# Optimization experiments

Hardware: AMD Instinct MI355X
Metric: run time of the kernel (lower is better)

## Reference

```python
import jax, jax.numpy as jnp
import numpy as np
import math

B, S, E, H = 4, 1024, 1024, 16
D = E // H
C = 1.0           # Poincare ball curvature
CS = math.sqrt(C)
EPS = 1e-7

def _sq(x):
    return jnp.sum(x * x, axis=-1, keepdims=True)

def expmap0(v):
    n = jnp.sqrt(jnp.clip(_sq(v), 1e-15))
    return jnp.tanh(CS * n) * v / (CS * n)

def logmap0(y):
    n = jnp.sqrt(jnp.clip(_sq(y), 1e-15))
    t = jnp.clip(CS * n, 0.0, 1.0 - 1e-6)
    return jnp.arctanh(t) * y / (CS * n)

def hlinear(x, z, r):
    # Poincare fully-connected layer (HNN++, Shimizu et al.), as in hypll HLinear
    lam = 2.0 / jnp.clip(1.0 - C * _sq(x), EPS)          # [..., 1] conformal factor
    zn = jnp.clip(jnp.linalg.norm(z, axis=0), 1e-15)     # [out]
    xz = x @ z                                           # [..., out]
    tcr = 2.0 * CS * r
    v = (2.0 * zn / CS) * jnp.arcsinh(CS * lam * xz / zn * jnp.cosh(tcr) - (lam - 1.0) * jnp.sinh(tcr))
    w = jnp.sinh(CS * v) / CS
    return w / (1.0 + jnp.sqrt(1.0 + C * jnp.sum(w * w, -1, keepdims=True)))

def _beta(a, b):
    return math.exp(math.lgamma(a) + math.lgamma(b) - math.lgamma(a + b))

def _forward(query, key, value, zq, bq, zk, bk, zv, bv):
    pq, pk, pv = hlinear(query, zq, bq), hlinear(key, zk, bk), hlinear(value, zv, bv)
    split = lambda x: x.reshape(B, S, H, D).transpose(0, 2, 1, 3)   # [B,H,S,D]
    q, k, v = split(pq), split(pk), split(pv)
    # attention_similarity: negative per-head pairwise Poincare distance (all heads vectorized)
    q2 = jnp.sum(q * q, -1)                              # [B,H,Sq]
    k2 = jnp.sum(k * k, -1)                              # [B,H,Sk]
    qk = jnp.einsum('bhqd,bhkd->bhqk', q, k)
    diff2 = jnp.clip(q2[..., :, None] + k2[..., None, :] - 2.0 * qk, 0.0)
    den = jnp.clip((1.0 - C * q2)[..., :, None] * (1.0 - C * k2)[..., None, :], EPS)
    dist = jnp.arccosh(jnp.clip(1.0 + 2.0 * C * diff2 / den, 1.0 + 1e-6)) / CS
    # attention_activation: softmax over keys
    w = jax.nn.softmax(-dist, axis=-1)                   # [B,H,Sq,Sk]
    # attention_midpoint: weighted gyromidpoint of values over keys
    lam = 2.0 / jnp.clip(1.0 - C * jnp.sum(v * v, -1), EPS)          # [B,H,Sk]
    num = jnp.einsum('bhqk,bhkd->bhqd', w * lam[..., None, :], v)
    dnm = jnp.clip(jnp.einsum('bhqk,bhk->bhq', jnp.abs(w), lam - 1.0), EPS)
    u = num / dnm[..., None]
    mid = u / (1.0 + jnp.sqrt(jnp.clip(1.0 - C * _sq(u), EPS)))      # (1/2) Mobius scalar mult
    # manifold.cat: beta-concatenation of heads (HNN++)
    scale = _beta(E / 2.0, 0.5) / _beta(D / 2.0, 0.5)
    tv = logmap0(mid) * scale                            # tangent at origin, [B,H,S,D]
    return expmap0(tv.transpose(0, 2, 1, 3).reshape(B, S, E))

def setup_inputs():
    key = jax.random.key(0)
    ks = jax.random.split(key, 9)
    mk = lambda k: expmap0(jax.random.normal(k, (B, S, E), jnp.float32) * (0.3 / math.sqrt(E)))
    zs = lambda k: jax.random.normal(k, (E, E), jnp.float32) / math.sqrt(E)
    bs = lambda k: jax.random.normal(k, (E,), jnp.float32) * 0.01
    return {"query": mk(ks[0]), "key": mk(ks[1]), "value": mk(ks[2]),
            "zq": zs(ks[3]), "bq": bs(ks[4]), "zk": zs(ks[5]), "bk": bs(ks[6]),
            "zv": zs(ks[7]), "bv": bs(ks[8])}

def reference(query, key, value, zq, bq, zk, bk, zv, bv):
    return _forward(query, key, value, zq, bq, zk, bk, zv, bv)
```

## Files before the change

### kernel.cpp

```cpp
#include <hip/hip_runtime.h>
#include <cmath>

#define EPSF 1e-7f

constexpr int B_ = 4, S_ = 1024, E_ = 1024, H_ = 16, D_ = 64;
constexpr int BS_ = B_ * S_;

typedef __attribute__((ext_vector_type(8))) short bf16x8;
typedef __attribute__((ext_vector_type(4))) float f32x4;

__device__ inline unsigned int fbits(float f) { union { float f; unsigned int u; } x; x.f = f; return x.u; }
__device__ inline float ubits(unsigned int u) { union { unsigned int u; float f; } x; x.u = u; return x.f; }

__device__ inline unsigned short f2bf(float f) {
  unsigned int u = fbits(f);
  unsigned int r = u + 0x7fffu + ((u >> 16) & 1u);
  return (unsigned short)(r >> 16);
}
__device__ inline float bf2f(unsigned short h) { return ubits(((unsigned int)h) << 16); }
__device__ inline float fastrcp(float x) { return __builtin_amdgcn_rcpf(x); }
__device__ inline float fastsqrt(float x) { return __builtin_amdgcn_sqrtf(x); }

__device__ __forceinline__ void async_ld16(const unsigned short* g, unsigned short* l) {
  __builtin_amdgcn_global_load_lds(
      (const __attribute__((address_space(1))) unsigned int*)g,
      (__attribute__((address_space(3))) unsigned int*)l, 16, 0, 0);
}

__device__ __forceinline__ unsigned int cvt_pk_bf16(float lo, float hi) {
  unsigned int r;
  asm("v_cvt_pk_bf16_f32 %0, %1, %2" : "=v"(r) : "v"(lo), "v"(hi));
  return r;
}
__device__ __forceinline__ void permlane32_swap(unsigned int &a, unsigned int &b) {
  asm("v_permlane32_swap_b32 %0, %1" : "+v"(a), "+v"(b));
}
__device__ __forceinline__ void permlane16_swap(unsigned int &a, unsigned int &b) {
  asm("v_permlane16_swap_b32 %0, %1" : "+v"(a), "+v"(b));
}

__global__ __launch_bounds__(256) void prep_kernel(
    const float* __restrict__ xq, const float* __restrict__ xk,
    const float* __restrict__ xv, unsigned short* __restrict__ Xbf,
    float* __restrict__ lamRow,
    const float* __restrict__ zq, const float* __restrict__ zk, const float* __restrict__ zv,
    unsigned short* __restrict__ BhiT, float* __restrict__ Zpart) {
  const int bid = blockIdx.x;
  const int tid = threadIdx.x;
  if (bid < 3 * BS_ / 4) {
    const int wid = tid >> 6, lane = tid & 63;
    const int row = bid * 4 + wid;
    const float* x = (row < BS_) ? xq : (row < 2 * BS_ ? xk : xv);
    const int r = row & (BS_ - 1);
    const float4* src = (const float4*)(x + (size_t)r * E_);
    float4 v[4];
    #pragma unroll
    for (int j = 0; j < 4; j++) v[j] = src[lane + 64 * j];
    float s = 0.f;
    #pragma unroll
    for (int j = 0; j < 4; j++)
      s += v[j].x * v[j].x + v[j].y * v[j].y + v[j].z * v[j].z + v[j].w * v[j].w;
    #pragma unroll
    for (int m = 1; m < 64; m <<= 1) s += __shfl_xor(s, m, 64);
    uint2* dst = (uint2*)(Xbf + (size_t)row * E_);
    #pragma unroll
    for (int j = 0; j < 4; j++) {
      uint2 p;
      p.x = (unsigned int)f2bf(v[j].x) | ((unsigned int)f2bf(v[j].y) << 16);
      p.y = (unsigned int)f2bf(v[j].z) | ((unsigned int)f2bf(v[j].w) << 16);
      dst[lane + 64 * j] = p;
    }
    if (lane == 0) lamRow[row] = 2.0f / fmaxf(1.0f - s, EPSF);
    return;
  }
  const int lid = bid - 3 * BS_ / 4;
  const int mat = lid >> 8;
  const int rem = lid & 255;
  const int ky = rem >> 4, nx = rem & 15;
  const float* z = mat == 0 ? zq : (mat == 1 ? zk : zv);
  const int k0 = ky * 64, n0 = nx * 64;
  __shared__ float t[64][65];
  __shared__ float sred[64][4];
  {
    int kr = tid >> 4, nc = (tid & 15) * 4;
    #pragma unroll
    for (int i = 0; i < 4; i++) {
      float4 vv = *(const float4*)(z + (size_t)(k0 + kr + i * 16) * E_ + n0 + nc);
      t[kr + i * 16][nc + 0] = vv.x;
      t[kr + i * 16][nc + 1] = vv.y;
      t[kr + i * 16][nc + 2] = vv.z;
      t[kr + i * 16][nc + 3] = vv.w;
    }
  }
  __syncthreads();
  int nr = tid >> 2, kc = (tid & 3) * 16;
  unsigned int ph[8];
  float ss = 0.f;
  #pragma unroll
  for (int p = 0; p < 8; p++) {
    float x0 = t[kc + 2 * p][nr], x1 = t[kc + 2 * p + 1][nr];
    ph[p] = (unsigned int)f2bf(x0) | ((unsigned int)f2bf(x1) << 16);
    ss += x0 * x0 + x1 * x1;
  }
  size_t off = (size_t)mat * E_ * E_ + (size_t)(n0 + nr) * E_ + k0 + kc;
  uint4* dh = (uint4*)(BhiT + off);
  dh[0] = make_uint4(ph[0], ph[1], ph[2], ph[3]);
  dh[1] = make_uint4(ph[4], ph[5], ph[6], ph[7]);
  sred[nr][tid & 3] = ss;
  __syncthreads();
  if (tid < 64) {
    float v = sred[tid][0] + sred[tid][1] + sred[tid][2] + sred[tid][3];
    Zpart[(size_t)(mat * 16 + ky) * E_ + n0 + tid] = v;
  }
}

__global__ __launch_bounds__(256, 3) void hlinear_mfma_kernel(
    const unsigned short* __restrict__ Xbf,
    const unsigned short* __restrict__ BhiT,
    const float* __restrict__ lamRow, const float* __restrict__ Zpart,
    const float* __restrict__ bq, const float* __restrict__ bk, const float* __restrict__ bv,
    unsigned short* __restrict__ Wbf) {
  const int fid = blockIdx.x;
  const int xcd = fid & 7, j = fid >> 3;
  const int n0 = (j & 7) * 128;
  const int gp = xcd * 12 + (j >> 3);
  const int mat = gp >> 5;
  const int m0 = (gp & 31) * 128;

  const unsigned short* xa = Xbf + (size_t)mat * BS_ * E_;
  const unsigned short* bh = BhiT + (size_t)mat * E_ * E_;

  __shared__ unsigned short LDSU[18432];
  __shared__ float chznS[128], shS[128], tznS[128];
  unsigned short* As = LDSU;
  unsigned short* Bh = LDSU + 8192;

  const int tid = threadIdx.x;
  const int wid = tid >> 6, lane = tid & 63, quad = lane >> 4, l16 = lane & 15;
  const int wm = (wid >> 1) * 64, wn = (wid & 1) * 64;

  if (tid < 128) {
    const int col = n0 + tid;
    float s = 0.f;
    #pragma unroll
    for (int ky = 0; ky < 16; ky++)
      s += Zpart[(size_t)(mat * 16 + ky) * E_ + col];
    float zn = fmaxf(sqrtf(s), 1e-15f);
    const float* bb = (mat == 0) ? bq : ((mat == 1) ? bk : bv);
    float rb = bb[col];
    chznS[tid] = coshf(2.f * rb) / zn;
    shS[tid] = sinhf(2.f * rb);
    tznS[tid] = 2.f * zn;
  }

  f32x4 acc[4][4];
  #pragma unroll
  for (int i = 0; i < 4; i++)
    #pragma unroll
    for (int jj = 0; jj < 4; jj++) acc[i][jj] = (f32x4){0.f, 0.f, 0.f, 0.f};

  const int lrow = lane >> 3;
  const int lcs = ((lane & 7) ^ lrow) * 8;
  const int xsw = (l16 & 7);

  for (int kt = 0; kt < E_ / 64; ++kt) {
    __syncthreads();
    const int kb = kt * 64 + lcs;
    #pragma unroll
    for (int c2 = 0; c2 < 4; c2++) {
      const int c = wid * 4 + c2;
      const int grow = c * 8 + lrow;
      async_ld16(xa + (size_t)(m0 + grow) * E_ + kb, As + c * 512);
      async_ld16(bh + (size_t)(n0 + grow) * E_ + kb, Bh + c * 512);
    }
    __syncthreads();
    #pragma unroll
    for (int h = 0; h < 2; h++) {
      bf16x8 a[4];
      #pragma unroll
      for (int mt = 0; mt < 4; mt++) {
        int row = wm + mt * 16 + l16;
        a[mt] = *(const bf16x8*)&As[row * 64 + (((h * 4 + quad) ^ xsw) * 8)];
      }
      #pragma unroll
      for (int nt = 0; nt < 4; nt++) {
        int row = wn + nt * 16 + l16;
        bf16x8 bhf = *(const bf16x8*)&Bh[row * 64 + (((h * 4 + quad) ^ xsw) * 8)];
        #pragma unroll
        for (int mt = 0; mt < 4; mt++)
          acc[mt][nt] = __builtin_amdgcn_mfma_f32_16x16x32_bf16(a[mt], bhf, acc[mt][nt], 0, 0, 0);
      }
    }
  }

  const float* lamP = lamRow + mat * BS_;
  float lamv[16];
  #pragma unroll
  for (int mt = 0; mt < 4; mt++)
    #pragma unroll
    for (int r = 0; r < 4; r++)
      lamv[mt * 4 + r] = lamP[m0 + wm + mt * 16 + quad * 4 + r];

  __syncthreads();
  unsigned short* epi = LDSU + wid * 4608;
  #pragma unroll
  for (int nt = 0; nt < 4; nt++) {
    int ci = wn + nt * 16 + l16;
    float chzn = chznS[ci];
    float sh = shS[ci];
    float tzn = tznS[ci];
    #pragma unroll
    for (int mt = 0; mt < 4; mt++) {
      #pragma unroll
      for (int r = 0; r < 4; r++) {
        float lam = lamv[mt * 4 + r];
        float arg = fmaf(lam * acc[mt][nt][r], chzn, -(lam - 1.f) * sh);
        float sq2 = sqrtf(fmaf(arg, arg, 1.f));
        float v = tzn * __logf(arg + sq2);
        float ev = __expf(v);
        float w = 0.5f * (ev - fastrcp(ev));
        epi[(mt * 16 + quad * 4 + r) * 72 + nt * 16 + l16] = f2bf(w);
      }
    }
  }
  unsigned short* gout = Wbf + (size_t)mat * BS_ * E_ + (size_t)(m0 + wm) * E_ + n0 + wn;
  const int rrow = lane >> 3, seg = lane & 7;
  #pragma unroll
  for (int i = 0; i < 8; i++) {
    int row = i * 8 + rrow;
    uint4 val = *(const uint4*)&epi[row * 72 + seg * 8];
    *(uint4*)(gout + (size_t)row * E_ + seg * 8) = val;
  }
}

__global__ __launch_bounds__(256) void normalize_kernel(
    const unsigned short* __restrict__ Wbf, unsigned short* __restrict__ Pbf,
    float* __restrict__ HN,
    unsigned short* __restrict__ KsG, unsigned short* __restrict__ lamMG,
    unsigned int* __restrict__ auxG) {
  const int wid = threadIdx.x >> 6, lane = threadIdx.x & 63;
  const int row = blockIdx.x * 4 + wid;
  const unsigned short* w = Wbf + (size_t)row * E_;
  union { uint4 q[2]; unsigned short s[16]; } in;
  in.q[0] = ((const uint4*)w)[lane * 2];
  in.q[1] = ((const uint4*)w)[lane * 2 + 1];
  float wv[16];
  float s = 0.f;
  #pragma unroll
  for (int i = 0; i < 16; i++) { wv[i] = bf2f(in.s[i]); s += wv[i] * wv[i]; }
  #pragma unroll
  for (int m = 1; m < 64; m <<= 1) s += __shfl_xor(s, m, 64);
  float t = 1.f / (1.f + sqrtf(1.f + s));
  union { uint4 q[2]; unsigned short s[16]; } out;
  float rv[16];
  float hs = 0.f;
  #pragma unroll
  for (int i = 0; i < 16; i++) {
    unsigned short p = f2bf(wv[i] * t);
    out.s[i] = p;
    rv[i] = bf2f(p);
    hs += rv[i] * rv[i];
  }
  hs += __shfl_xor(hs, 1, 64);
  hs += __shfl_xor(hs, 2, 64);
  const int mat = row >= 2 * BS_ ? 2 : (row >= BS_ ? 1 : 0);
  const int r4 = row & (BS_ - 1);
  const int b = r4 >> 10, key = r4 & (S_ - 1);
  const int head = lane >> 2;
  const size_t bhS = ((size_t)(b * H_ + head)) * S_;
  if (mat == 0) {
    ((uint4*)(Pbf + (size_t)row * E_))[lane * 2] = out.q[0];
    ((uint4*)(Pbf + (size_t)row * E_))[lane * 2 + 1] = out.q[1];
    if ((lane & 3) == 0) HN[(size_t)r4 * H_ + head] = hs;
  } else if (mat == 1) {
    float c = fastrcp(1.f - hs);
    union { uint4 q[2]; unsigned short s[16]; } ks;
    #pragma unroll
    for (int i = 0; i < 16; i++) ks.s[i] = f2bf(rv[i] * c);
    unsigned short* dst = KsG + (bhS + key) * 64 + (lane & 3) * 16;
    ((uint4*)dst)[0] = ks.q[0];
    ((uint4*)dst)[1] = ks.q[1];
    if ((lane & 3) == 0)
      auxG[bhS + key] = (unsigned int)f2bf(c) | ((unsigned int)f2bf(c * hs) << 16);
  } else {
    float lam = 2.f / fmaxf(1.f - hs, EPSF);
    union { uint4 q[2]; unsigned short s[16]; } pv;
    #pragma unroll
    for (int i = 0; i < 16; i++) pv.s[i] = f2bf(rv[i] * lam);
    ((uint4*)(Pbf + (size_t)row * E_))[lane * 2] = pv.q[0];
    ((uint4*)(Pbf + (size_t)row * E_))[lane * 2 + 1] = pv.q[1];
    if ((lane & 3) == 0) lamMG[bhS + key] = f2bf(lam - 1.f);
  }
}

__global__ __launch_bounds__(256) void vtrans_kernel(
    const unsigned short* __restrict__ PvF, unsigned short* __restrict__ VtG) {
  const int st = blockIdx.x, h = blockIdx.y, b = blockIdx.z;
  __shared__ unsigned short T[64][72];
  const int tid = threadIdx.x;
  const size_t bhS = (size_t)(b * H_ + h) * S_;
  {
    int lr = tid >> 2, lc = (tid & 3) * 16;
    const uint4* src = (const uint4*)(PvF + (size_t)(b * S_ + st * 64 + lr) * E_ + h * 64 + lc);
    *(uint4*)&T[lr][lc] = src[0];
    *(uint4*)&T[lr][lc + 8] = src[1];
  }
  __syncthreads();
  int d = tid >> 2, sc = (tid & 3) * 16;
  unsigned int o[8];
  #pragma unroll
  for (int i = 0; i < 8; i++) {
    int s0 = sc + 2 * i;
    o[i] = (unsigned int)T[s0][d] | ((unsigned int)T[s0 + 1][d] << 16);
  }
  unsigned short* dst = VtG + bhS * 64 + (size_t)d * S_ + st * 64 + sc;
  ((uint4*)dst)[0] = make_uint4(o[0], o[1], o[2], o[3]);
  ((uint4*)dst)[1] = make_uint4(o[4], o[5], o[6], o[7]);
}

__global__ __launch_bounds__(512) void attention_kernel(
    const unsigned short* __restrict__ Pbf, const float* __restrict__ HN,
    const unsigned short* __restrict__ KsG, const unsigned short* __restrict__ VtG,
    const unsigned short* __restrict__ lamMG, const unsigned int* __restrict__ auxG,
    float* __restrict__ TV, float scale) {
  const int fid = blockIdx.x;
  const int xcd = fid & 7, slot = fid >> 3;
  const int group = xcd + 8 * (slot >> 3);
  const int qt = slot & 7;
  const int h = group & 15, b = group >> 4;

  const unsigned short* pq = Pbf;
  const float* hnq = HN;

  const int tid = threadIdx.x;
  const int wid = tid >> 6, lane = tid & 63;
  const int quad = lane >> 4, l16 = lane & 15;

  __shared__ __align__(16) unsigned short Kl[2][8192];
  __shared__ __align__(16) unsigned short Vl[2][8192];
  __shared__ __align__(16) unsigned short lamL[1024];
  __shared__ __align__(16) unsigned int auxL[1024];

  const size_t bhS = (size_t)(b * H_ + h) * S_;
  const int lr = lane >> 3, cch = lane & 7;
  const int xsw = l16 & 7;
  const unsigned short* kbase = KsG + bhS * 64;
  const unsigned short* vbase = VtG + bhS * 64;
  const int srow = wid * 8 + lr;
  const int scc = ((cch ^ lr) * 8);

  async_ld16(kbase + (size_t)srow * 64 + scc, &Kl[0][wid * 512]);
  async_ld16(kbase + (size_t)(64 + srow) * 64 + scc, &Kl[0][4096 + wid * 512]);
  async_ld16(vbase + (size_t)srow * S_ + scc, &Vl[0][wid * 512]);
  async_ld16(vbase + (size_t)srow * S_ + 64 + scc, &Vl[0][4096 + wid * 512]);

  ((unsigned int*)lamL)[tid] = ((const unsigned int*)(lamMG + bhS))[tid];
  ((uint2*)auxL)[tid] = ((const uint2*)(auxG + bhS))[tid];

  const int qrow0 = qt * 128 + wid * 16;
  const size_t qgrow = ((size_t)(b * S_ + qrow0 + l16)) * E_ + h * 64;
  bf16x8 aq0r = *(const bf16x8*)(pq + qgrow + quad * 8);
  bf16x8 aq1r = *(const bf16x8*)(pq + qgrow + 32 + quad * 8);
  const float q2l = hnq[((size_t)(b * S_ + qrow0 + l16)) * H_ + h];
  const float al = 2.f * fastrcp(1.f - q2l);
  const float sc2 = -2.f * al;
  bf16x8 aq0, aq1;
  #pragma unroll
  for (int j = 0; j < 8; j++) {
    aq0[j] = (short)f2bf(bf2f((unsigned short)aq0r[j]) * sc2);
    aq1[j] = (short)f2bf(bf2f((unsigned short)aq1r[j]) * sc2);
  }
  const unsigned short ae0 = (quad == 0) ? f2bf(al * q2l) : 0;
  const unsigned short ae1 = (quad == 0) ? f2bf(al) : 0;
  const bf16x8 aex = (bf16x8){(short)ae0, (short)ae1, 0, 0, 0, 0, 0, 0};

  f32x4 accO[4];
  #pragma unroll
  for (int dt = 0; dt < 4; dt++) accO[dt] = (f32x4){0.f, 0.f, 0.f, 0.f};
  f32x4 accD = (f32x4){0.f, 0.f, 0.f, 0.f};

  asm volatile("s_waitcnt vmcnt(0) lgkmcnt(0)" ::: "memory");
  __builtin_amdgcn_s_barrier();

  const int NIT = S_ / 128;
  int buf = 0;
  #pragma unroll 1
  for (int it = 0; it < NIT; ++it) {
    if (it + 1 < NIT) {
      const int kr0 = (it + 1) * 128;
      async_ld16(kbase + (size_t)(kr0 + srow) * 64 + scc, &Kl[buf ^ 1][wid * 512]);
      async_ld16(kbase + (size_t)(kr0 + 64 + srow) * 64 + scc, &Kl[buf ^ 1][4096 + wid * 512]);
      async_ld16(vbase + (size_t)srow * S_ + kr0 + scc, &Vl[buf ^ 1][wid * 512]);
      async_ld16(vbase + (size_t)srow * S_ + kr0 + 64 + scc, &Vl[buf ^ 1][4096 + wid * 512]);
    }
    #pragma unroll
    for (int half = 0; half < 2; half++) {
      const int kt = it * 2 + half;
      const unsigned short* Kb = &Kl[buf][half * 4096];
      const unsigned short* Vb = &Vl[buf][half * 4096];

      unsigned int Wp[4][2];
      #pragma unroll
      for (int nt = 0; nt < 4; nt++) {
        const int krow = nt * 16 + l16;
        bf16x8 bk0 = *(const bf16x8*)&Kb[krow * 64 + ((quad ^ xsw) * 8)];
        bf16x8 bk1 = *(const bf16x8*)&Kb[krow * 64 + (((4 + quad) ^ xsw) * 8)];
        unsigned int av = (quad == 0) ? auxL[kt * 64 + krow] : 0u;
        bf16x8 bex = (bf16x8){(short)(av & 0xFFFF), (short)(av >> 16), 0, 0, 0, 0, 0, 0};
        f32x4 z = (f32x4){0.f, 0.f, 0.f, 0.f};
        f32x4 st = __builtin_amdgcn_mfma_f32_16x16x32_bf16(bex, aex, z, 0, 0, 0);
        st = __builtin_amdgcn_mfma_f32_16x16x32_bf16(bk0, aq0, st, 0, 0, 0);
        st = __builtin_amdgcn_mfma_f32_16x16x32_bf16(bk1, aq1, st, 0, 0, 0);
        float w[4];
        #pragma unroll
        for (int r2 = 0; r2 < 4; r2++) {
          float t = fmaxf(st[r2], 1e-6f);
          float A = 1.f + t;
          w[r2] = A - fastsqrt(fmaf(A, A, -1.f));
        }
        Wp[nt][0] = cvt_pk_bf16(w[0], w[1]);
        Wp[nt][1] = cvt_pk_bf16(w[2], w[3]);
      }
      unsigned int x00 = Wp[0][0], y00 = Wp[1][0];
      permlane32_swap(x00, y00); permlane16_swap(x00, y00);
      unsigned int x01 = Wp[0][1], y01 = Wp[1][1];
      permlane32_swap(x01, y01); permlane16_swap(x01, y01);
      unsigned int x10 = Wp[2][0], y10 = Wp[3][0];
      permlane32_swap(x10, y10); permlane16_swap(x10, y10);
      unsigned int x11 = Wp[2][1], y11 = Wp[3][1];
      permlane32_swap(x11, y11); permlane16_swap(x11, y11);
      union { unsigned int u[4]; bf16x8 v; } ap0u, ap1u;
      ap0u.u[0] = x00; ap0u.u[1] = x01; ap0u.u[2] = y00; ap0u.u[3] = y01;
      ap1u.u[0] = x10; ap1u.u[1] = x11; ap1u.u[2] = y10; ap1u.u[3] = y11;
      const bf16x8 ap0 = ap0u.v, ap1 = ap1u.v;

      #pragma unroll
      for (int dt = 0; dt < 4; dt++) {
        const int drow = dt * 16 + l16;
        bf16x8 bv0 = *(const bf16x8*)&Vb[drow * 64 + ((quad ^ xsw) * 8)];
        bf16x8 bv1 = *(const bf16x8*)&Vb[drow * 64 + (((4 + quad) ^ xsw) * 8)];
        accO[dt] = __builtin_amdgcn_mfma_f32_16x16x32_bf16(ap0, bv0, accO[dt], 0, 0, 0);
        accO[dt] = __builtin_amdgcn_mfma_f32_16x16x32_bf16(ap1, bv1, accO[dt], 0, 0, 0);
      }
      bf16x8 bl0 = *(const bf16x8*)&lamL[kt * 64 + quad * 8];
      bf16x8 bl1 = *(const bf16x8*)&lamL[kt * 64 + 32 + quad * 8];
      accD = __builtin_amdgcn_mfma_f32_16x16x32_bf16(ap0, bl0, accD, 0, 0, 0);
      accD = __builtin_amdgcn_mfma_f32_16x16x32_bf16(ap1, bl1, accD, 0, 0, 0);
    }

    asm volatile("s_waitcnt vmcnt(0)" ::: "memory");
    __builtin_amdgcn_s_barrier();
    buf ^= 1;
  }

  #pragma unroll
  for (int r2 = 0; r2 < 4; r2++) {
    float rdsum = fastrcp(accD[r2]);
    float uu[4];
    float su = 0.f;
    #pragma unroll
    for (int dt = 0; dt < 4; dt++) { uu[dt] = accO[dt][r2] * rdsum; su += uu[dt] * uu[dt]; }
    su += __shfl_xor(su, 1, 64);
    su += __shfl_xor(su, 2, 64);
    su += __shfl_xor(su, 4, 64);
    su += __shfl_xor(su, 8, 64);
    float g = fastrcp(1.f + fastsqrt(fmaxf(1.f - su, EPSF)));
    float n2 = fmaxf(su * g * g, 1e-15f);
    float n = fastsqrt(n2);
    float fac = atanhf(fminf(n, 1.f - 1e-6f)) * fastrcp(n) * g * scale;
    size_t orow = ((size_t)(b * S_ + qrow0 + quad * 4 + r2)) * E_ + h * 64 + l16;
    #pragma unroll
    for (int dt = 0; dt < 4; dt++) TV[orow + dt * 16] = fac * uu[dt];
  }
}

__global__ __launch_bounds__(256) void expmap_kernel(float* __restrict__ TV) {
  const int wid = threadIdx.x >> 6, lane = threadIdx.x & 63;
  const int row = blockIdx.x * 4 + wid;
  float* w = TV + (size_t)row * E_;
  float4 v[4];
  #pragma unroll
  for (int j = 0; j < 4; j++) v[j] = ((float4*)w)[lane + 64 * j];
  float s = 0.f;
  #pragma unroll
  for (int j = 0; j < 4; j++)
    s += v[j].x * v[j].x + v[j].y * v[j].y + v[j].z * v[j].z + v[j].w * v[j].w;
  #pragma unroll
  for (int m = 1; m < 64; m <<= 1) s += __shfl_xor(s, m, 64);
  float n = sqrtf(fmaxf(s, 1e-15f));
  float f = tanhf(n) / n;
  #pragma unroll
  for (int j = 0; j < 4; j++) {
    v[j].x *= f; v[j].y *= f; v[j].z *= f; v[j].w *= f;
    ((float4*)w)[lane + 64 * j] = v[j];
  }
}

extern "C" void kernel_launch(void* const* d_in, const int* in_sizes, int n_in,
                              void* d_out, int out_size, void* d_ws, size_t ws_size,
                              hipStream_t stream) {
  (void)in_sizes; (void)n_in; (void)out_size; (void)ws_size;
  const float* q  = (const float*)d_in[0];
  const float* k  = (const float*)d_in[1];
  const float* v  = (const float*)d_in[2];
  const float* zq = (const float*)d_in[3];
  const float* bq = (const float*)d_in[4];
  const float* zk = (const float*)d_in[5];
  const float* bk = (const float*)d_in[6];
  const float* zv = (const float*)d_in[7];
  const float* bv = (const float*)d_in[8];

  unsigned short* Wbf = (unsigned short*)d_ws;
  unsigned short* Pbf = Wbf + (size_t)3 * BS_ * E_;
  unsigned short* BhiT = Pbf;
  unsigned short* Xbf = Pbf + (size_t)3 * BS_ * E_;
  float* HN           = (float*)(Xbf + (size_t)3 * BS_ * E_);
  float* lamRow       = HN + (size_t)3 * BS_ * H_;
  float* Zpart        = lamRow + 3 * BS_;
  unsigned short* VtG = (unsigned short*)(Zpart + 48 * E_);
  unsigned short* KsG = VtG + (size_t)B_ * H_ * 64 * S_;
  unsigned short* lamMG = KsG + (size_t)B_ * H_ * S_ * 64;
  unsigned int* auxG  = (unsigned int*)(lamMG + (size_t)B_ * H_ * S_);
  unsigned short* PvF = Pbf + (size_t)2 * BS_ * E_;
  float* out          = (float*)d_out;

  double lb1 = lgamma(E_ / 2.0) + lgamma(0.5) - lgamma(E_ / 2.0 + 0.5);
  double lb2 = lgamma(D_ / 2.0) + lgamma(0.5) - lgamma(D_ / 2.0 + 0.5);
  float scale = (float)exp(lb1 - lb2);

  hipLaunchKernelGGL(prep_kernel, dim3(3 * BS_ / 4 + 768), dim3(256), 0, stream,
                     q, k, v, Xbf, lamRow, zq, zk, zv, BhiT, Zpart);
  hipLaunchKernelGGL(hlinear_mfma_kernel, dim3(768), dim3(256), 0, stream,
                     Xbf, BhiT, lamRow, Zpart, bq, bk, bv, Wbf);
  hipLaunchKernelGGL(normalize_kernel, dim3(3 * BS_ / 4), dim3(256), 0, stream,
                     Wbf, Pbf, HN, KsG, lamMG, auxG);
  hipLaunchKernelGGL(vtrans_kernel, dim3(16, 16, 4), dim3(256), 0, stream, PvF, VtG);
  hipLaunchKernelGGL(attention_kernel, dim3(512), dim3(512), 0, stream,
                     Pbf, HN, KsG, VtG, lamMG, auxG, out, scale);
  hipLaunchKernelGGL(expmap_kernel, dim3(BS_ / 4), dim3(256), 0, stream, out);
}
```

Baseline: 214.9 us.

## Restructure attention to 4 waves with 32 query rows per wave

Each attention block now runs 4 waves instead of 8, and each wave handles two 16-row query subtiles, so every K/V fragment read from LDS is reused for both subtiles. The key tile shrinks from 128 to 64 per iteration, which halves the double-buffered LDS footprint, and launch bounds ask for two blocks per CU. s_setprio is raised around the PV MFMA section to favor matrix issue. The aim is fewer LDS reads per MFMA and better latency hiding across co-resident blocks, at the cost of higher register pressure and twice as many barrier iterations.

```diff
diff --git a/kernel.cpp b/kernel.cpp
--- a/kernel.cpp
+++ b/kernel.cpp
@@ -318,7 +318,7 @@
   ((uint4*)dst)[1] = make_uint4(o[4], o[5], o[6], o[7]);
 }
 
-__global__ __launch_bounds__(512) void attention_kernel(
+__global__ __launch_bounds__(256, 2) void attention_kernel(
     const unsigned short* __restrict__ Pbf, const float* __restrict__ HN,
     const unsigned short* __restrict__ KsG, const unsigned short* __restrict__ VtG,
     const unsigned short* __restrict__ lamMG, const unsigned int* __restrict__ auxG,
@@ -336,8 +336,8 @@
   const int wid = tid >> 6, lane = tid & 63;
   const int quad = lane >> 4, l16 = lane & 15;
 
-  __shared__ __align__(16) unsigned short Kl[2][8192];
-  __shared__ __align__(16) unsigned short Vl[2][8192];
+  __shared__ __align__(16) unsigned short Kl[2][4096];
+  __shared__ __align__(16) unsigned short Vl[2][4096];
   __shared__ __align__(16) unsigned short lamL[1024];
   __shared__ __align__(16) unsigned int auxL[1024];
 
@@ -346,71 +346,80 @@
   const int xsw = l16 & 7;
   const unsigned short* kbase = KsG + bhS * 64;
   const unsigned short* vbase = VtG + bhS * 64;
-  const int srow = wid * 8 + lr;
   const int scc = ((cch ^ lr) * 8);
 
-  async_ld16(kbase + (size_t)srow * 64 + scc, &Kl[0][wid * 512]);
-  async_ld16(kbase + (size_t)(64 + srow) * 64 + scc, &Kl[0][4096 + wid * 512]);
-  async_ld16(vbase + (size_t)srow * S_ + scc, &Vl[0][wid * 512]);
-  async_ld16(vbase + (size_t)srow * S_ + 64 + scc, &Vl[0][4096 + wid * 512]);
-
-  ((unsigned int*)lamL)[tid] = ((const unsigned int*)(lamMG + bhS))[tid];
-  ((uint2*)auxL)[tid] = ((const uint2*)(auxG + bhS))[tid];
-
-  const int qrow0 = qt * 128 + wid * 16;
-  const size_t qgrow = ((size_t)(b * S_ + qrow0 + l16)) * E_ + h * 64;
-  bf16x8 aq0r = *(const bf16x8*)(pq + qgrow + quad * 8);
-  bf16x8 aq1r = *(const bf16x8*)(pq + qgrow + 32 + quad * 8);
-  const float q2l = hnq[((size_t)(b * S_ + qrow0 + l16)) * H_ + h];
-  const float al = 2.f * fastrcp(1.f - q2l);
-  const float sc2 = -2.f * al;
-  bf16x8 aq0, aq1;
-  #pragma unroll
-  for (int j = 0; j < 8; j++) {
-    aq0[j] = (short)f2bf(bf2f((unsigned short)aq0r[j]) * sc2);
-    aq1[j] = (short)f2bf(bf2f((unsigned short)aq1r[j]) * sc2);
-  }
-  const unsigned short ae0 = (quad == 0) ? f2bf(al * q2l) : 0;
-  const unsigned short ae1 = (quad == 0) ? f2bf(al) : 0;
-  const bf16x8 aex = (bf16x8){(short)ae0, (short)ae1, 0, 0, 0, 0, 0, 0};
-
-  f32x4 accO[4];
-  #pragma unroll
-  for (int dt = 0; dt < 4; dt++) accO[dt] = (f32x4){0.f, 0.f, 0.f, 0.f};
-  f32x4 accD = (f32x4){0.f, 0.f, 0.f, 0.f};
+  #pragma unroll
+  for (int i = 0; i < 2; i++) {
+    const int srow = i * 32 + wid * 8 + lr;
+    async_ld16(kbase + (size_t)srow * 64 + scc, &Kl[0][i * 2048 + wid * 512]);
+    async_ld16(vbase + (size_t)srow * S_ + scc, &Vl[0][i * 2048 + wid * 512]);
+  }
+
+  ((uint2*)lamL)[tid] = ((const uint2*)(lamMG + bhS))[tid];
+  ((uint4*)auxL)[tid] = ((const uint4*)(auxG + bhS))[tid];
+
+  const int qrow0 = qt * 128 + wid * 32;
+  bf16x8 aq0[2], aq1[2], aex[2];
+  #pragma unroll
+  for (int s = 0; s < 2; s++) {
+    const int qr = qrow0 + s * 16 + l16;
+    const size_t qgrow = ((size_t)(b * S_ + qr)) * E_ + h * 64;
+    bf16x8 a0r = *(const bf16x8*)(pq + qgrow + quad * 8);
+    bf16x8 a1r = *(const bf16x8*)(pq + qgrow + 32 + quad * 8);
+    const float q2l = hnq[((size_t)(b * S_ + qr)) * H_ + h];
+    const float al = 2.f * fastrcp(1.f - q2l);
+    const float sc2 = -2.f * al;
+    #pragma unroll
+    for (int j = 0; j < 8; j++) {
+      aq0[s][j] = (short)f2bf(bf2f((unsigned short)a0r[j]) * sc2);
+      aq1[s][j] = (short)f2bf(bf2f((unsigned short)a1r[j]) * sc2);
+    }
+    const unsigned short ae0 = (quad == 0) ? f2bf(al * q2l) : 0;
+    const unsigned short ae1 = (quad == 0) ? f2bf(al) : 0;
+    aex[s] = (bf16x8){(short)ae0, (short)ae1, 0, 0, 0, 0, 0, 0};
+  }
+
+  f32x4 accO[2][4];
+  f32x4 accD[2];
+  #pragma unroll
+  for (int s = 0; s < 2; s++) {
+    #pragma unroll
+    for (int dt = 0; dt < 4; dt++) accO[s][dt] = (f32x4){0.f, 0.f, 0.f, 0.f};
+    accD[s] = (f32x4){0.f, 0.f, 0.f, 0.f};
+  }
 
   asm volatile("s_waitcnt vmcnt(0) lgkmcnt(0)" ::: "memory");
   __builtin_amdgcn_s_barrier();
 
-  const int NIT = S_ / 128;
+  const int NT = S_ / 64;
   int buf = 0;
   #pragma unroll 1
-  for (int it = 0; it < NIT; ++it) {
-    if (it + 1 < NIT) {
-      const int kr0 = (it + 1) * 128;
-      async_ld16(kbase + (size_t)(kr0 + srow) * 64 + scc, &Kl[buf ^ 1][wid * 512]);
-      async_ld16(kbase + (size_t)(kr0 + 64 + srow) * 64 + scc, &Kl[buf ^ 1][4096 + wid * 512]);
-      async_ld16(vbase + (size_t)srow * S_ + kr0 + scc, &Vl[buf ^ 1][wid * 512]);
-      async_ld16(vbase + (size_t)srow * S_ + kr0 + 64 + scc, &Vl[buf ^ 1][4096 + wid * 512]);
-    }
-    #pragma unroll
-    for (int half = 0; half < 2; half++) {
-      const int kt = it * 2 + half;
-      const unsigned short* Kb = &Kl[buf][half * 4096];
-      const unsigned short* Vb = &Vl[buf][half * 4096];
-
-      unsigned int Wp[4][2];
-      #pragma unroll
-      for (int nt = 0; nt < 4; nt++) {
-        const int krow = nt * 16 + l16;
-        bf16x8 bk0 = *(const bf16x8*)&Kb[krow * 64 + ((quad ^ xsw) * 8)];
-        bf16x8 bk1 = *(const bf16x8*)&Kb[krow * 64 + (((4 + quad) ^ xsw) * 8)];
-        unsigned int av = (quad == 0) ? auxL[kt * 64 + krow] : 0u;
-        bf16x8 bex = (bf16x8){(short)(av & 0xFFFF), (short)(av >> 16), 0, 0, 0, 0, 0, 0};
+  for (int kt = 0; kt < NT; ++kt) {
+    if (kt + 1 < NT) {
+      #pragma unroll
+      for (int i = 0; i < 2; i++) {
+        const int srow = i * 32 + wid * 8 + lr;
+        async_ld16(kbase + (size_t)((kt + 1) * 64 + srow) * 64 + scc, &Kl[buf ^ 1][i * 2048 + wid * 512]);
+        async_ld16(vbase + (size_t)(srow * S_ + (kt + 1) * 64) + scc, &Vl[buf ^ 1][i * 2048 + wid * 512]);
+      }
+    }
+    const unsigned short* Kb = Kl[buf];
+    const unsigned short* Vb = Vl[buf];
+
+    unsigned int Wp[2][4][2];
+    #pragma unroll
+    for (int nt = 0; nt < 4; nt++) {
+      const int krow = nt * 16 + l16;
+      bf16x8 bk0 = *(const bf16x8*)&Kb[krow * 64 + ((quad ^ xsw) * 8)];
+      bf16x8 bk1 = *(const bf16x8*)&Kb[krow * 64 + (((4 + quad) ^ xsw) * 8)];
+      unsigned int av = (quad == 0) ? auxL[kt * 64 + krow] : 0u;
+      bf16x8 bex = (bf16x8){(short)(av & 0xFFFF), (short)(av >> 16), 0, 0, 0, 0, 0, 0};
+      #pragma unroll
+      for (int s = 0; s < 2; s++) {
         f32x4 z = (f32x4){0.f, 0.f, 0.f, 0.f};
-        f32x4 st = __builtin_amdgcn_mfma_f32_16x16x32_bf16(bex, aex, z, 0, 0, 0);
-        st = __builtin_amdgcn_mfma_f32_16x16x32_bf16(bk0, aq0, st, 0, 0, 0);
-        st = __builtin_amdgcn_mfma_f32_16x16x32_bf16(bk1, aq1, st, 0, 0, 0);
+        f32x4 st = __builtin_amdgcn_mfma_f32_16x16x32_bf16(bex, aex[s], z, 0, 0, 0);
+        st = __builtin_amdgcn_mfma_f32_16x16x32_bf16(bk0, aq0[s], st, 0, 0, 0);
+        st = __builtin_amdgcn_mfma_f32_16x16x32_bf16(bk1, aq1[s], st, 0, 0, 0);
         float w[4];
         #pragma unroll
         for (int r2 = 0; r2 < 4; r2++) {
@@ -418,35 +427,49 @@
           float A = 1.f + t;
           w[r2] = A - fastsqrt(fmaf(A, A, -1.f));
         }
-        Wp[nt][0] = cvt_pk_bf16(w[0], w[1]);
-        Wp[nt][1] = cvt_pk_bf16(w[2], w[3]);
-      }
-      unsigned int x00 = Wp[0][0], y00 = Wp[1][0];
+        Wp[s][nt][0] = cvt_pk_bf16(w[0], w[1]);
+        Wp[s][nt][1] = cvt_pk_bf16(w[2], w[3]);
+      }
+    }
+    bf16x8 ap0[2], ap1[2];
+    #pragma unroll
+    for (int s = 0; s < 2; s++) {
+      unsigned int x00 = Wp[s][0][0], y00 = Wp[s][1][0];
       permlane32_swap(x00, y00); permlane16_swap(x00, y00);
-      unsigned int x01 = Wp[0][1], y01 = Wp[1][1];
+      unsigned int x01 = Wp[s][0][1], y01 = Wp[s][1][1];
       permlane32_swap(x01, y01); permlane16_swap(x01, y01);
-      unsigned int x10 = Wp[2][0], y10 = Wp[3][0];
+      unsigned int x10 = Wp[s][2][0], y10 = Wp[s][3][0];
       permlane32_swap(x10, y10); permlane16_swap(x10, y10);
-      unsigned int x11 = Wp[2][1], y11 = Wp[3][1];
+      unsigned int x11 = Wp[s][2][1], y11 = Wp[s][3][1];
       permlane32_swap(x11, y11); permlane16_swap(x11, y11);
       union { unsigned int u[4]; bf16x8 v; } ap0u, ap1u;
       ap0u.u[0] = x00; ap0u.u[1] = x01; ap0u.u[2] = y00; ap0u.u[3] = y01;
       ap1u.u[0] = x10; ap1u.u[1] = x11; ap1u.u[2] = y10; ap1u.u[3] = y11;
-      const bf16x8 ap0 = ap0u.v, ap1 = ap1u.v;
-
-      #pragma unroll
-      for (int dt = 0; dt < 4; dt++) {
-        const int drow = dt * 16 + l16;
-        bf16x8 bv0 = *(const bf16x8*)&Vb[drow * 64 + ((quad ^ xsw) * 8)];
-        bf16x8 bv1 = *(const bf16x8*)&Vb[drow * 64 + (((4 + quad) ^ xsw) * 8)];
-        accO[dt] = __builtin_amdgcn_mfma_f32_16x16x32_bf16(ap0, bv0, accO[dt], 0, 0, 0);
-        accO[dt] = __builtin_amdgcn_mfma_f32_16x16x32_bf16(ap1, bv1, accO[dt], 0, 0, 0);
-      }
+      ap0[s] = ap0u.v; ap1[s] = ap1u.v;
+    }
+
+    __builtin_amdgcn_s_setprio(1);
+    #pragma unroll
+    for (int dt = 0; dt < 4; dt++) {
+      const int drow = dt * 16 + l16;
+      bf16x8 bv0 = *(const bf16x8*)&Vb[drow * 64 + ((quad ^ xsw) * 8)];
+      bf16x8 bv1 = *(const bf16x8*)&Vb[drow * 64 + (((4 + quad) ^ xsw) * 8)];
+      #pragma unroll
+      for (int s = 0; s < 2; s++) {
+        accO[s][dt] = __builtin_amdgcn_mfma_f32_16x16x32_bf16(ap0[s], bv0, accO[s][dt], 0, 0, 0);
+        accO[s][dt] = __builtin_amdgcn_mfma_f32_16x16x32_bf16(ap1[s], bv1, accO[s][dt], 0, 0, 0);
+      }
+    }
+    {
       bf16x8 bl0 = *(const bf16x8*)&lamL[kt * 64 + quad * 8];
       bf16x8 bl1 = *(const bf16x8*)&lamL[kt * 64 + 32 + quad * 8];
-      accD = __builtin_amdgcn_mfma_f32_16x16x32_bf16(ap0, bl0, accD, 0, 0, 0);
-      accD = __builtin_amdgcn_mfma_f32_16x16x32_bf16(ap1, bl1, accD, 0, 0, 0);
-    }
+      #pragma unroll
+      for (int s = 0; s < 2; s++) {
+        accD[s] = __builtin_amdgcn_mfma_f32_16x16x32_bf16(ap0[s], bl0, accD[s], 0, 0, 0);
+        accD[s] = __builtin_amdgcn_mfma_f32_16x16x32_bf16(ap1[s], bl1, accD[s], 0, 0, 0);
+      }
+    }
+    __builtin_amdgcn_s_setprio(0);
 
     asm volatile("s_waitcnt vmcnt(0)" ::: "memory");
     __builtin_amdgcn_s_barrier();
@@ -454,23 +477,26 @@
   }
 
   #pragma unroll
-  for (int r2 = 0; r2 < 4; r2++) {
-    float rdsum = fastrcp(accD[r2]);
-    float uu[4];
-    float su = 0.f;
-    #pragma unroll
-    for (int dt = 0; dt < 4; dt++) { uu[dt] = accO[dt][r2] * rdsum; su += uu[dt] * uu[dt]; }
-    su += __shfl_xor(su, 1, 64);
-    su += __shfl_xor(su, 2, 64);
-    su += __shfl_xor(su, 4, 64);
-    su += __shfl_xor(su, 8, 64);
-    float g = fastrcp(1.f + fastsqrt(fmaxf(1.f - su, EPSF)));
-    float n2 = fmaxf(su * g * g, 1e-15f);
-    float n = fastsqrt(n2);
-    float fac = atanhf(fminf(n, 1.f - 1e-6f)) * fastrcp(n) * g * scale;
-    size_t orow = ((size_t)(b * S_ + qrow0 + quad * 4 + r2)) * E_ + h * 64 + l16;
-    #pragma unroll
-    for (int dt = 0; dt < 4; dt++) TV[orow + dt * 16] = fac * uu[dt];
+  for (int s = 0; s < 2; s++) {
+    #pragma unroll
+    for (int r2 = 0; r2 < 4; r2++) {
+      float rdsum = fastrcp(accD[s][r2]);
+      float uu[4];
+      float su = 0.f;
+      #pragma unroll
+      for (int dt = 0; dt < 4; dt++) { uu[dt] = accO[s][dt][r2] * rdsum; su += uu[dt] * uu[dt]; }
+      su += __shfl_xor(su, 1, 64);
+      su += __shfl_xor(su, 2, 64);
+      su += __shfl_xor(su, 4, 64);
+      su += __shfl_xor(su, 8, 64);
+      float g = fastrcp(1.f + fastsqrt(fmaxf(1.f - su, EPSF)));
+      float n2 = fmaxf(su * g * g, 1e-15f);
+      float n = fastsqrt(n2);
+      float fac = atanhf(fminf(n, 1.f - 1e-6f)) * fastrcp(n) * g * scale;
+      size_t orow = ((size_t)(b * S_ + qrow0 + s * 16 + quad * 4 + r2)) * E_ + h * 64 + l16;
+      #pragma unroll
+      for (int dt = 0; dt < 4; dt++) TV[orow + dt * 16] = fac * uu[dt];
+    }
   }
 }
 
@@ -535,7 +561,7 @@
   hipLaunchKernelGGL(normalize_kernel, dim3(3 * BS_ / 4), dim3(256), 0, stream,
                      Wbf, Pbf, HN, KsG, lamMG, auxG);
   hipLaunchKernelGGL(vtrans_kernel, dim3(16, 16, 4), dim3(256), 0, stream, PvF, VtG);
-  hipLaunchKernelGGL(attention_kernel, dim3(512), dim3(512), 0, stream,
+  hipLaunchKernelGGL(attention_kernel, dim3(512), dim3(256), 0, stream,
                      Pbf, HN, KsG, VtG, lamMG, auxG, out, scale);
   hipLaunchKernelGGL(expmap_kernel, dim3(BS_ / 4), dim3(256), 0, stream, out);
 }
```

Result: no change. 215.9 us (+0.4%).

## Double-buffer LDS tiles in hlinear GEMM to overlap loads with MFMA

Applied to the files above, without the earlier changes.

The hlinear MFMA kernel now uses two LDS buffers. It prefetches the next K tile with async global-to-LDS loads while the current tile feeds the MFMAs, so only one barrier per iteration is needed instead of two. LDS use grows to 64KB per block, and the launch bound drops from 3 to 2 blocks per CU, which reduces occupancy. The s_waitcnt vmcnt(0) sits after the compute, so the load latency can be hidden behind the MFMA work.

```diff
diff --git a/kernel.cpp b/kernel.cpp
--- a/kernel.cpp
+++ b/kernel.cpp
@@ -114,7 +114,7 @@
   }
 }
 
-__global__ __launch_bounds__(256, 3) void hlinear_mfma_kernel(
+__global__ __launch_bounds__(256, 2) void hlinear_mfma_kernel(
     const unsigned short* __restrict__ Xbf,
     const unsigned short* __restrict__ BhiT,
     const float* __restrict__ lamRow, const float* __restrict__ Zpart,
@@ -130,14 +130,24 @@
   const unsigned short* xa = Xbf + (size_t)mat * BS_ * E_;
   const unsigned short* bh = BhiT + (size_t)mat * E_ * E_;
 
-  __shared__ unsigned short LDSU[18432];
+  __shared__ unsigned short LDSU[2][16384];
   __shared__ float chznS[128], shS[128], tznS[128];
-  unsigned short* As = LDSU;
-  unsigned short* Bh = LDSU + 8192;
 
   const int tid = threadIdx.x;
   const int wid = tid >> 6, lane = tid & 63, quad = lane >> 4, l16 = lane & 15;
   const int wm = (wid >> 1) * 64, wn = (wid & 1) * 64;
+
+  const int lrow = lane >> 3;
+  const int lcs = ((lane & 7) ^ lrow) * 8;
+  const int xsw = (l16 & 7);
+
+  #pragma unroll
+  for (int c2 = 0; c2 < 4; c2++) {
+    const int c = wid * 4 + c2;
+    const int grow = c * 8 + lrow;
+    async_ld16(xa + (size_t)(m0 + grow) * E_ + lcs, &LDSU[0][c * 512]);
+    async_ld16(bh + (size_t)(n0 + grow) * E_ + lcs, &LDSU[0][8192 + c * 512]);
+  }
 
   if (tid < 128) {
     const int col = n0 + tid;
@@ -159,21 +169,25 @@
     #pragma unroll
     for (int jj = 0; jj < 4; jj++) acc[i][jj] = (f32x4){0.f, 0.f, 0.f, 0.f};
 
-  const int lrow = lane >> 3;
-  const int lcs = ((lane & 7) ^ lrow) * 8;
-  const int xsw = (l16 & 7);
-
-  for (int kt = 0; kt < E_ / 64; ++kt) {
-    __syncthreads();
-    const int kb = kt * 64 + lcs;
-    #pragma unroll
-    for (int c2 = 0; c2 < 4; c2++) {
-      const int c = wid * 4 + c2;
-      const int grow = c * 8 + lrow;
-      async_ld16(xa + (size_t)(m0 + grow) * E_ + kb, As + c * 512);
-      async_ld16(bh + (size_t)(n0 + grow) * E_ + kb, Bh + c * 512);
-    }
-    __syncthreads();
+  asm volatile("s_waitcnt vmcnt(0) lgkmcnt(0)" ::: "memory");
+  __builtin_amdgcn_s_barrier();
+
+  const int NTk = E_ / 64;
+  int buf = 0;
+  #pragma unroll 1
+  for (int kt = 0; kt < NTk; ++kt) {
+    if (kt + 1 < NTk) {
+      const int kb = (kt + 1) * 64 + lcs;
+      #pragma unroll
+      for (int c2 = 0; c2 < 4; c2++) {
+        const int c = wid * 4 + c2;
+        const int grow = c * 8 + lrow;
+        async_ld16(xa + (size_t)(m0 + grow) * E_ + kb, &LDSU[buf ^ 1][c * 512]);
+        async_ld16(bh + (size_t)(n0 + grow) * E_ + kb, &LDSU[buf ^ 1][8192 + c * 512]);
+      }
+    }
+    const unsigned short* As = LDSU[buf];
+    const unsigned short* Bh2 = LDSU[buf] + 8192;
     #pragma unroll
     for (int h = 0; h < 2; h++) {
       bf16x8 a[4];
@@ -185,12 +199,15 @@
       #pragma unroll
       for (int nt = 0; nt < 4; nt++) {
         int row = wn + nt * 16 + l16;
-        bf16x8 bhf = *(const bf16x8*)&Bh[row * 64 + (((h * 4 + quad) ^ xsw) * 8)];
+        bf16x8 bhf = *(const bf16x8*)&Bh2[row * 64 + (((h * 4 + quad) ^ xsw) * 8)];
         #pragma unroll
         for (int mt = 0; mt < 4; mt++)
           acc[mt][nt] = __builtin_amdgcn_mfma_f32_16x16x32_bf16(a[mt], bhf, acc[mt][nt], 0, 0, 0);
       }
     }
+    asm volatile("s_waitcnt vmcnt(0)" ::: "memory");
+    __builtin_amdgcn_s_barrier();
+    buf ^= 1;
   }
 
   const float* lamP = lamRow + mat * BS_;
@@ -202,7 +219,7 @@
       lamv[mt * 4 + r] = lamP[m0 + wm + mt * 16 + quad * 4 + r];
 
   __syncthreads();
-  unsigned short* epi = LDSU + wid * 4608;
+  unsigned short* epi = &LDSU[0][0] + wid * 4608;
   #pragma unroll
   for (int nt = 0; nt < 4; nt++) {
     int ci = wn + nt * 16 + l16;
```

Measured after the change: 217.4 us. Within noise of the previous version (+1.1%).

## Fuse value normalization into V transpose kernel, dropping a launch and intermediate

Applied to the files above, without the earlier changes.

Merges the normalize and V-transpose kernels into one launch. Q/K rows are handled as before. V tiles are normalized inside the transpose blocks, which recompute each row's full norm from the raw hlinear output, then scale by the conformal factor and write the transposed result. This removes the PvF write/read round trip and a kernel launch. In exchange, each V row is re-read by all 16 head blocks to compute its norm, and the XCD-aware block mapping is meant to keep those re-reads in L2.

```diff
diff --git a/kernel.cpp b/kernel.cpp
--- a/kernel.cpp
+++ b/kernel.cpp
@@ -233,89 +233,122 @@
   }
 }
 
-__global__ __launch_bounds__(256) void normalize_kernel(
+__global__ __launch_bounds__(256) void norm_vtrans_kernel(
     const unsigned short* __restrict__ Wbf, unsigned short* __restrict__ Pbf,
     float* __restrict__ HN,
     unsigned short* __restrict__ KsG, unsigned short* __restrict__ lamMG,
-    unsigned int* __restrict__ auxG) {
-  const int wid = threadIdx.x >> 6, lane = threadIdx.x & 63;
-  const int row = blockIdx.x * 4 + wid;
-  const unsigned short* w = Wbf + (size_t)row * E_;
-  union { uint4 q[2]; unsigned short s[16]; } in;
-  in.q[0] = ((const uint4*)w)[lane * 2];
-  in.q[1] = ((const uint4*)w)[lane * 2 + 1];
-  float wv[16];
-  float s = 0.f;
-  #pragma unroll
-  for (int i = 0; i < 16; i++) { wv[i] = bf2f(in.s[i]); s += wv[i] * wv[i]; }
-  #pragma unroll
-  for (int m = 1; m < 64; m <<= 1) s += __shfl_xor(s, m, 64);
-  float t = 1.f / (1.f + sqrtf(1.f + s));
-  union { uint4 q[2]; unsigned short s[16]; } out;
-  float rv[16];
-  float hs = 0.f;
-  #pragma unroll
-  for (int i = 0; i < 16; i++) {
-    unsigned short p = f2bf(wv[i] * t);
-    out.s[i] = p;
-    rv[i] = bf2f(p);
-    hs += rv[i] * rv[i];
-  }
-  hs += __shfl_xor(hs, 1, 64);
-  hs += __shfl_xor(hs, 2, 64);
-  const int mat = row >= 2 * BS_ ? 2 : (row >= BS_ ? 1 : 0);
-  const int r4 = row & (BS_ - 1);
-  const int b = r4 >> 10, key = r4 & (S_ - 1);
-  const int head = lane >> 2;
-  const size_t bhS = ((size_t)(b * H_ + head)) * S_;
-  if (mat == 0) {
-    ((uint4*)(Pbf + (size_t)row * E_))[lane * 2] = out.q[0];
-    ((uint4*)(Pbf + (size_t)row * E_))[lane * 2 + 1] = out.q[1];
-    if ((lane & 3) == 0) HN[(size_t)r4 * H_ + head] = hs;
-  } else if (mat == 1) {
-    float c = fastrcp(1.f - hs);
-    union { uint4 q[2]; unsigned short s[16]; } ks;
-    #pragma unroll
-    for (int i = 0; i < 16; i++) ks.s[i] = f2bf(rv[i] * c);
-    unsigned short* dst = KsG + (bhS + key) * 64 + (lane & 3) * 16;
-    ((uint4*)dst)[0] = ks.q[0];
-    ((uint4*)dst)[1] = ks.q[1];
-    if ((lane & 3) == 0)
-      auxG[bhS + key] = (unsigned int)f2bf(c) | ((unsigned int)f2bf(c * hs) << 16);
-  } else {
-    float lam = 2.f / fmaxf(1.f - hs, EPSF);
-    union { uint4 q[2]; unsigned short s[16]; } pv;
-    #pragma unroll
-    for (int i = 0; i < 16; i++) pv.s[i] = f2bf(rv[i] * lam);
-    ((uint4*)(Pbf + (size_t)row * E_))[lane * 2] = pv.q[0];
-    ((uint4*)(Pbf + (size_t)row * E_))[lane * 2 + 1] = pv.q[1];
-    if ((lane & 3) == 0) lamMG[bhS + key] = f2bf(lam - 1.f);
-  }
-}
-
-__global__ __launch_bounds__(256) void vtrans_kernel(
-    const unsigned short* __restrict__ PvF, unsigned short* __restrict__ VtG) {
-  const int st = blockIdx.x, h = blockIdx.y, b = blockIdx.z;
+    unsigned int* __restrict__ auxG, unsigned short* __restrict__ VtG) {
+  const int bid = blockIdx.x;
+  const int tid = threadIdx.x;
+  if (bid < 2 * BS_ / 4) {
+    const int wid = tid >> 6, lane = tid & 63;
+    const int row = bid * 4 + wid;
+    const unsigned short* w = Wbf + (size_t)row * E_;
+    union { uint4 q[2]; unsigned short s[16]; } in;
+    in.q[0] = ((const uint4*)w)[lane * 2];
+    in.q[1] = ((const uint4*)w)[lane * 2 + 1];
+    float wv[16];
+    float s = 0.f;
+    #pragma unroll
+    for (int i = 0; i < 16; i++) { wv[i] = bf2f(in.s[i]); s += wv[i] * wv[i]; }
+    #pragma unroll
+    for (int m = 1; m < 64; m <<= 1) s += __shfl_xor(s, m, 64);
+    float t = 1.f / (1.f + sqrtf(1.f + s));
+    union { uint4 q[2]; unsigned short s[16]; } out;
+    float rv[16];
+    float hs = 0.f;
+    #pragma unroll
+    for (int i = 0; i < 16; i++) {
+      unsigned short p = f2bf(wv[i] * t);
+      out.s[i] = p;
+      rv[i] = bf2f(p);
+      hs += rv[i] * rv[i];
+    }
+    hs += __shfl_xor(hs, 1, 64);
+    hs += __shfl_xor(hs, 2, 64);
+    const int mat = row >= BS_ ? 1 : 0;
+    const int r4 = row & (BS_ - 1);
+    const int b = r4 >> 10, key = r4 & (S_ - 1);
+    const int head = lane >> 2;
+    const size_t bhS = ((size_t)(b * H_ + head)) * S_;
+    if (mat == 0) {
+      ((uint4*)(Pbf + (size_t)row * E_))[lane * 2] = out.q[0];
+      ((uint4*)(Pbf + (size_t)row * E_))[lane * 2 + 1] = out.q[1];
+      if ((lane & 3) == 0) HN[(size_t)r4 * H_ + head] = hs;
+    } else {
+      float c = fastrcp(1.f - hs);
+      union { uint4 q[2]; unsigned short s[16]; } ks;
+      #pragma unroll
+      for (int i = 0; i < 16; i++) ks.s[i] = f2bf(rv[i] * c);
+      unsigned short* dst = KsG + (bhS + key) * 64 + (lane & 3) * 16;
+      ((uint4*)dst)[0] = ks.q[0];
+      ((uint4*)dst)[1] = ks.q[1];
+      if ((lane & 3) == 0)
+        auxG[bhS + key] = (unsigned int)f2bf(c) | ((unsigned int)f2bf(c * hs) << 16);
+    }
+    return;
+  }
+  const int lid = bid - 2 * BS_ / 4;
+  const int xcd = lid & 7, s2 = lid >> 3;
+  const int g = xcd + 8 * (s2 >> 4);
+  const int h = s2 & 15;
+  const int b = g >> 4, st = g & 15;
+  const unsigned short* wvbase = Wbf + (size_t)2 * BS_ * E_;
   __shared__ unsigned short T[64][72];
-  const int tid = threadIdx.x;
-  const size_t bhS = (size_t)(b * H_ + h) * S_;
+  __shared__ float tS[64];
+  const int wid = tid >> 6, lane = tid & 63;
+  #pragma unroll 1
+  for (int kk = 0; kk < 16; ++kk) {
+    const int key = wid * 16 + kk;
+    const unsigned short* rowp = wvbase + (size_t)(b * S_ + st * 64 + key) * E_;
+    union { uint4 q[2]; unsigned short s[16]; } in;
+    in.q[0] = ((const uint4*)rowp)[lane * 2];
+    in.q[1] = ((const uint4*)rowp)[lane * 2 + 1];
+    float s = 0.f;
+    #pragma unroll
+    for (int i = 0; i < 16; i++) { float f = bf2f(in.s[i]); s += f * f; }
+    #pragma unroll
+    for (int m = 1; m < 64; m <<= 1) s += __shfl_xor(s, m, 64);
+    if ((lane >> 2) == h) {
+      *(uint4*)&T[key][(lane & 3) * 16] = in.q[0];
+      *(uint4*)&T[key][(lane & 3) * 16 + 8] = in.q[1];
+    }
+    if (lane == 0) tS[key] = 1.f / (1.f + sqrtf(1.f + s));
+  }
+  __syncthreads();
   {
-    int lr = tid >> 2, lc = (tid & 3) * 16;
-    const uint4* src = (const uint4*)(PvF + (size_t)(b * S_ + st * 64 + lr) * E_ + h * 64 + lc);
-    *(uint4*)&T[lr][lc] = src[0];
-    *(uint4*)&T[lr][lc + 8] = src[1];
+    const int kr = tid >> 2, lc = (tid & 3) * 16;
+    const float t = tS[kr];
+    float rv[16];
+    float hp = 0.f;
+    #pragma unroll
+    for (int i = 0; i < 16; i++) {
+      unsigned short p = f2bf(bf2f(T[kr][lc + i]) * t);
+      rv[i] = bf2f(p);
+      hp += rv[i] * rv[i];
+    }
+    hp += __shfl_xor(hp, 1, 64);
+    hp += __shfl_xor(hp, 2, 64);
+    float lam = 2.f / fmaxf(1.f - hp, EPSF);
+    #pragma unroll
+    for (int i = 0; i < 16; i++) T[kr][lc + i] = f2bf(rv[i] * lam);
+    const size_t bhS = ((size_t)(b * H_ + h)) * S_;
+    if ((tid & 3) == 0) lamMG[bhS + st * 64 + kr] = f2bf(lam - 1.f);
   }
   __syncthreads();
-  int d = tid >> 2, sc = (tid & 3) * 16;
-  unsigned int o[8];
-  #pragma unroll
-  for (int i = 0; i < 8; i++) {
-    int s0 = sc + 2 * i;
-    o[i] = (unsigned int)T[s0][d] | ((unsigned int)T[s0 + 1][d] << 16);
-  }
-  unsigned short* dst = VtG + bhS * 64 + (size_t)d * S_ + st * 64 + sc;
-  ((uint4*)dst)[0] = make_uint4(o[0], o[1], o[2], o[3]);
-  ((uint4*)dst)[1] = make_uint4(o[4], o[5], o[6], o[7]);
+  {
+    const int d = tid >> 2, sc = (tid & 3) * 16;
+    unsigned int o[8];
+    #pragma unroll
+    for (int i = 0; i < 8; i++) {
+      int s0 = sc + 2 * i;
+      o[i] = (unsigned int)T[s0][d] | ((unsigned int)T[s0 + 1][d] << 16);
+    }
+    const size_t bhS = ((size_t)(b * H_ + h)) * S_;
+    unsigned short* dst = VtG + bhS * 64 + (size_t)d * S_ + st * 64 + sc;
+    ((uint4*)dst)[0] = make_uint4(o[0], o[1], o[2], o[3]);
+    ((uint4*)dst)[1] = make_uint4(o[4], o[5], o[6], o[7]);
+  }
 }
 
 __global__ __launch_bounds__(512) void attention_kernel(
@@ -521,7 +554,6 @@
   unsigned short* KsG = VtG + (size_t)B_ * H_ * 64 * S_;
   unsigned short* lamMG = KsG + (size_t)B_ * H_ * S_ * 64;
   unsigned int* auxG  = (unsigned int*)(lamMG + (size_t)B_ * H_ * S_);
-  unsigned short* PvF = Pbf + (size_t)2 * BS_ * E_;
   float* out          = (float*)d_out;
 
   double lb1 = lgamma(E_ / 2.0) + lgamma(0.5) - lgamma(E_ / 2.0 + 0.5);
@@ -532,9 +564,8 @@
                      q, k, v, Xbf, lamRow, zq, zk, zv, BhiT, Zpart);
   hipLaunchKernelGGL(hlinear_mfma_kernel, dim3(768), dim3(256), 0, stream,
                      Xbf, BhiT, lamRow, Zpart, bq, bk, bv, Wbf);
-  hipLaunchKernelGGL(normalize_kernel, dim3(3 * BS_ / 4), dim3(256), 0, stream,
-                     Wbf, Pbf, HN, KsG, lamMG, auxG);
-  hipLaunchKernelGGL(vtrans_kernel, dim3(16, 16, 4), dim3(256), 0, stream, PvF, VtG);
+  hipLaunchKernelGGL(norm_vtrans_kernel, dim3(2 * BS_ / 4 + 1024), dim3(256), 0, stream,
+                     Wbf, Pbf, HN, KsG, lamMG, auxG, VtG);
   hipLaunchKernelGGL(attention_kernel, dim3(512), dim3(512), 0, stream,
                      Pbf, HN, KsG, VtG, lamMG, auxG, out, scale);
   hipLaunchKernelGGL(expmap_kernel, dim3(BS_ / 4), dim3(256), 0, stream, out);
```

New measurement: 216.3 us (median of 2 runs). About the same (+0.6%).
